# Optimization experiments

Hardware: AMD Instinct MI355X
Metric: run time of the kernel (lower is better)

Reference implementation:

```python
import jax, jax.numpy as jnp
import numpy as np

B, Tq, DIM = 4, 2048, 1024
TKV, N_LAT, DLAT = 16, 64, 1024
HEADS, DHEAD = 8, 64
LN_EPS = 1e-5


def setup_inputs() -> dict:
    key = jax.random.key(0)
    ks = jax.random.split(key, 6)
    qo = jax.random.normal(ks[0], (B, Tq, DIM), dtype=jnp.float32)
    kvo = jax.random.normal(ks[1], (B, TKV, N_LAT, DLAT), dtype=jnp.float32)
    # 16 media tokens, evenly spaced, first at index 16 (so q_time==0 for early tokens)
    media = jnp.zeros((B, Tq), dtype=bool)
    idx = 16 + jnp.arange(TKV) * (Tq // TKV)  # 16, 144, ..., 1936
    media = media.at[:, idx].set(True)
    ln_g = jnp.ones((DIM,), dtype=jnp.float32)
    ln_b = jnp.zeros((DIM,), dtype=jnp.float32)
    Wq = jax.random.normal(ks[2], (DIM, HEADS * DHEAD), dtype=jnp.float32) * 0.02
    Wkv = jax.random.normal(ks[3], (DLAT, HEADS * DHEAD * 2), dtype=jnp.float32) * 0.02
    Wout = jax.random.normal(ks[4], (HEADS * DHEAD, DIM), dtype=jnp.float32) * 0.02
    return {"qo": qo, "kvo": kvo, "media_locations": media,
            "ln_g": ln_g, "ln_b": ln_b, "Wq": Wq, "Wkv": Wkv, "Wout": Wout}


def _layernorm(x, g, b):
    mu = jnp.mean(x, axis=-1, keepdims=True)
    var = jnp.var(x, axis=-1, keepdims=True)
    return (x - mu) * jax.lax.rsqrt(var + LN_EPS) * g + b


def reference(qo, kvo, media_locations, ln_g, ln_b, Wq, Wkv, Wout):
    scale = DHEAD ** (-0.5)
    b, tq, _ = qo.shape
    _, tkv, n, _ = kvo.shape
    q = _layernorm(qo, ln_g, ln_b) @ Wq  # (b, tq, h*d)
    q = q.reshape(b, tq, HEADS, DHEAD).transpose(0, 2, 1, 3) * scale  # b h i d
    kv = kvo.reshape(b, tkv * n, -1) @ Wkv  # (b, j, 2*h*d)
    k, v = jnp.split(kv, 2, axis=-1)
    k = k.reshape(b, tkv * n, HEADS, DHEAD).transpose(0, 2, 1, 3)  # b h j d
    v = v.reshape(b, tkv * n, HEADS, DHEAD).transpose(0, 2, 1, 3)
    sim = jnp.einsum('bhid,bhjd->bhij', q, k)  # (b, h, tq, tkv*n)
    kv_time = jnp.repeat(jnp.arange(tkv) + 1, n)  # (tkv*n,)
    q_time = jnp.cumsum(media_locations.astype(jnp.int32), axis=-1)  # (b, tq)
    mask = q_time[:, None, :, None] == kv_time[None, None, None, :]  # only_attend_immediate
    neg = -jnp.finfo(sim.dtype).max
    sim = jnp.where(mask, sim, neg)
    attn = jax.nn.softmax(sim, axis=-1)
    attn = jnp.where((q_time == 0)[:, None, :, None], 0.0, attn)
    out = jnp.einsum('bhij,bhjd->bhid', attn, v)
    out = out.transpose(0, 2, 1, 3).reshape(b, tq, HEADS * DHEAD)
    return out @ Wout
```

## Files before the change

kernel.cpp:

```cpp
#include <hip/hip_runtime.h>
#include <cstdint>
#include <cstddef>

#define BB    4
#define TQ    2048
#define DIM   1024
#define TKV   16
#define NLAT  64
#define DLAT  1024
#define HEADS 8
#define DHEAD 64
#define LN_EPS 1e-5f
#define NKV   (TKV*NLAT)
#define HD    (HEADS*DHEAD)

typedef unsigned short u16;
typedef __bf16 bf16x8 __attribute__((ext_vector_type(8)));
typedef float  f32x4  __attribute__((ext_vector_type(4)));

__device__ __forceinline__ u16 f2bf(float f) {
    unsigned u = __builtin_bit_cast(unsigned, f);
    u += 0x7fffu + ((u >> 16) & 1u);
    return (u16)(u >> 16);
}
__device__ __forceinline__ void gl_lds16(const void* g, void* l) {
    __builtin_amdgcn_global_load_lds(
        (const __attribute__((address_space(1))) void*)g,
        (__attribute__((address_space(3))) void*)l, 16, 0, 0);
}

__device__ __forceinline__ void transpose_dev(const float* __restrict__ W,
                                              u16* __restrict__ Wt,
                                              int K, int N, int n0, int k0,
                                              float (*tile)[33]) {
    int t = threadIdx.x;
    int r = t >> 3, c4 = (t & 7) * 4;
    float4 v = *(const float4*)&W[(size_t)(k0 + r) * N + n0 + c4];
    tile[r][c4 + 0] = v.x; tile[r][c4 + 1] = v.y;
    tile[r][c4 + 2] = v.z; tile[r][c4 + 3] = v.w;
    __syncthreads();
    uint2 pk;
    pk.x = (unsigned)f2bf(tile[c4 + 0][r]) | ((unsigned)f2bf(tile[c4 + 1][r]) << 16);
    pk.y = (unsigned)f2bf(tile[c4 + 2][r]) | ((unsigned)f2bf(tile[c4 + 3][r]) << 16);
    *(uint2*)&Wt[(size_t)(n0 + r) * K + k0 + c4] = pk;
}

__global__ __launch_bounds__(256) void prep_k(
    const float* __restrict__ qo, const float* __restrict__ kvo,
    const uint8_t* __restrict__ media,
    const float* __restrict__ ln_g, const float* __restrict__ ln_b,
    const float* __restrict__ Wq, const float* __restrict__ Wkv,
    const float* __restrict__ Wout,
    int* __restrict__ qt, u16* __restrict__ Aq, u16* __restrict__ Akv,
    u16* __restrict__ Wqt, u16* __restrict__ Wkvt, u16* __restrict__ Woutt) {
    __shared__ int part[256];
    __shared__ int cnt_sh;
    __shared__ float sh[8];
    __shared__ float mu_s, rs_s;
    __shared__ float tile[32][33];
    int blk = blockIdx.x, t = threadIdx.x;

    if (blk < 4) {
        int b = blk;
        int c = 0;
        for (int i = 0; i < 32; ++i) c += (media[t * 32 + i] != 0);
        part[t] = c;
        __syncthreads();
        if (t == 0) { int s = 0; for (int i = 0; i < 256; ++i) s += part[i]; cnt_sh = s; }
        __syncthreads();
        bool is_u8 = (cnt_sh >= 48);
        int vals[8];
        for (int i = 0; i < 8; ++i) {
            int idx = t * 8 + i;
            int m;
            if (is_u8) m = (media[(size_t)b * TQ + idx] != 0) ? 1 : 0;
            else       m = (((const uint32_t*)media)[(size_t)b * TQ + idx] != 0u) ? 1 : 0;
            vals[i] = m;
        }
        int loc = 0;
        for (int i = 0; i < 8; ++i) loc += vals[i];
        __syncthreads();
        part[t] = loc;
        __syncthreads();
        int pre = 0;
        for (int i = 0; i < t; ++i) pre += part[i];
        int run = pre;
        for (int i = 0; i < 8; ++i) {
            run += vals[i];
            qt[(size_t)b * TQ + t * 8 + i] = run;
        }
    } else if (blk < 4 + BB * TQ) {
        int row = blk - 4;
        float4 v = *(const float4*)(qo + (size_t)row * DIM + t * 4);
        float s  = v.x + v.y + v.z + v.w;
        float ss = v.x * v.x + v.y * v.y + v.z * v.z + v.w * v.w;
        for (int off = 32; off; off >>= 1) { s += __shfl_down(s, off); ss += __shfl_down(ss, off); }
        if ((t & 63) == 0) { sh[(t >> 6) * 2] = s; sh[(t >> 6) * 2 + 1] = ss; }
        __syncthreads();
        if (t == 0) {
            float S  = sh[0] + sh[2] + sh[4] + sh[6];
            float SS = sh[1] + sh[3] + sh[5] + sh[7];
            float m  = S * (1.0f / DIM);
            mu_s = m;
            rs_s = rsqrtf(SS * (1.0f / DIM) - m * m + LN_EPS);
        }
        __syncthreads();
        float mu = mu_s, rs = rs_s;
        float4 gv = *(const float4*)(ln_g + t * 4);
        float4 bv = *(const float4*)(ln_b + t * 4);
        float a0 = (v.x - mu) * rs * gv.x + bv.x;
        float a1 = (v.y - mu) * rs * gv.y + bv.y;
        float a2 = (v.z - mu) * rs * gv.z + bv.z;
        float a3 = (v.w - mu) * rs * gv.w + bv.w;
        uint2 pk;
        pk.x = (unsigned)f2bf(a0) | ((unsigned)f2bf(a1) << 16);
        pk.y = (unsigned)f2bf(a2) | ((unsigned)f2bf(a3) << 16);
        *(uint2*)(Aq + (size_t)row * DIM + t * 4) = pk;
    } else if (blk < 4 + BB * TQ + 2048) {
        size_t i = (size_t)(blk - 4 - BB * TQ) * 256 + t;
        float4 a = ((const float4*)kvo)[i * 2];
        float4 b = ((const float4*)kvo)[i * 2 + 1];
        uint4 pk;
        pk.x = (unsigned)f2bf(a.x) | ((unsigned)f2bf(a.y) << 16);
        pk.y = (unsigned)f2bf(a.z) | ((unsigned)f2bf(a.w) << 16);
        pk.z = (unsigned)f2bf(b.x) | ((unsigned)f2bf(b.y) << 16);
        pk.w = (unsigned)f2bf(b.z) | ((unsigned)f2bf(b.w) << 16);
        ((uint4*)Akv)[i] = pk;
    } else if (blk < 10244 + 512) {
        int id = blk - 10244;
        transpose_dev(Wq, Wqt, DIM, HD, (id & 15) * 32, (id >> 4) * 32, tile);
    } else if (blk < 10756 + 1024) {
        int id = blk - 10756;
        transpose_dev(Wkv, Wkvt, DLAT, 2 * HD, (id & 31) * 32, (id >> 5) * 32, tile);
    } else {
        int id = blk - 11780;
        transpose_dev(Wout, Woutt, HD, DIM, (id & 31) * 32, (id >> 5) * 32, tile);
    }
}

template <typename CT>
__device__ __forceinline__ void gemm_body(const u16* __restrict__ A,
                                          const u16* __restrict__ Bt,
                                          CT* __restrict__ C,
                                          int M, int N, int K, float outscale,
                                          int bx, int by,
                                          u16* As0, u16* Bs0, u16* As1, u16* Bs1) {
    int t = threadIdx.x;
    int lane = t & 63, w = t >> 6;
    int wr = w >> 1, wc = w & 1;
    int fr = lane & 15, fg = lane >> 4;
    int row0 = by * 128, col0 = bx * 128;

    const u16* Ag = A  + (size_t)(row0 + (t >> 2)) * K + (t & 3) * 8;
    const u16* Bg = Bt + (size_t)(col0 + (t >> 2)) * K + (t & 3) * 8;
    size_t rstr = (size_t)64 * K;

    int aoff = (wr * 64 + fr) * 32 + fg * 8;
    int boff = (wc * 64 + fr) * 32 + fg * 8;

    f32x4 acc[4][4];
#pragma unroll
    for (int mi = 0; mi < 4; ++mi)
#pragma unroll
        for (int ni = 0; ni < 4; ++ni) acc[mi][ni] = (f32x4){0.f, 0.f, 0.f, 0.f};

    auto stage = [&](u16* Asb, u16* Bsb, int k0) {
        char* al = (char*)Asb + w * 1024;
        char* bl = (char*)Bsb + w * 1024;
        gl_lds16(Ag + k0,        al);
        gl_lds16(Ag + k0 + rstr, al + 4096);
        gl_lds16(Bg + k0,        bl);
        gl_lds16(Bg + k0 + rstr, bl + 4096);
    };
    auto compute = [&](const u16* Asb, const u16* Bsb) {
        bf16x8 af[4], bfv[4];
#pragma unroll
        for (int mi = 0; mi < 4; ++mi) af[mi]  = *(const bf16x8*)(Asb + aoff + mi * 512);
#pragma unroll
        for (int ni = 0; ni < 4; ++ni) bfv[ni] = *(const bf16x8*)(Bsb + boff + ni * 512);
#pragma unroll
        for (int mi = 0; mi < 4; ++mi)
#pragma unroll
            for (int ni = 0; ni < 4; ++ni)
                acc[mi][ni] = __builtin_amdgcn_mfma_f32_16x16x32_bf16(
                    af[mi], bfv[ni], acc[mi][ni], 0, 0, 0);
    };

    int nt = K >> 5;
    stage(As0, Bs0, 0);
    __syncthreads();
    for (int it = 0; it < nt; it += 2) {
        stage(As1, Bs1, (it + 1) << 5);
        compute(As0, Bs0);
        __syncthreads();
        if (it + 2 < nt) stage(As0, Bs0, (it + 2) << 5);
        compute(As1, Bs1);
        __syncthreads();
    }

#pragma unroll
    for (int mi = 0; mi < 4; ++mi) {
        int r0 = row0 + wr * 64 + mi * 16 + fg * 4;
#pragma unroll
        for (int ni = 0; ni < 4; ++ni) {
            int c = col0 + wc * 64 + ni * 16 + fr;
#pragma unroll
            for (int j = 0; j < 4; ++j) {
                float val = acc[mi][ni][j] * outscale;
                if constexpr (sizeof(CT) == 2) C[(size_t)(r0 + j) * N + c] = f2bf(val);
                else                           C[(size_t)(r0 + j) * N + c] = val;
            }
        }
    }
}

__global__ __launch_bounds__(256) void proj_k(
    const u16* __restrict__ Aq,  const u16* __restrict__ Wqt,  u16* __restrict__ qb,
    const u16* __restrict__ Akv, const u16* __restrict__ Wkvt, u16* __restrict__ kvb) {
    __shared__ u16 As0[4096], Bs0[4096], As1[4096], Bs1[4096];
    int id = blockIdx.x;
    if (id < 256) {
        gemm_body<u16>(Aq, Wqt, qb, BB * TQ, HD, DIM, 0.125f, id & 3, id >> 2,
                       As0, Bs0, As1, Bs1);
    } else {
        id -= 256;
        gemm_body<u16>(Akv, Wkvt, kvb, BB * NKV, 2 * HD, DLAT, 1.0f, id & 7, id >> 3,
                       As0, Bs0, As1, Bs1);
    }
}

__global__ __launch_bounds__(256) void out_k(
    const u16* __restrict__ aob, const u16* __restrict__ Woutt, float* __restrict__ out) {
    __shared__ u16 As0[4096], Bs0[4096], As1[4096], Bs1[4096];
    int id = blockIdx.x;
    gemm_body<float>(aob, Woutt, out, BB * TQ, DIM, HD, 1.0f, id & 7, id >> 3,
                     As0, Bs0, As1, Bs1);
}

__global__ __launch_bounds__(256) void attn_k(
    const u16* __restrict__ q,
    const u16* __restrict__ kv,
    const int* __restrict__ qt,
    u16* __restrict__ ao) {
    __shared__ u16 Ks[4096];
    __shared__ u16 VT[4096];
    __shared__ u16 Ps[1024];
    __shared__ float redm[4][16], reds[4][16];
    int i0 = blockIdx.x * 16;
    int h  = blockIdx.y;
    int b  = blockIdx.z;
    int t  = threadIdx.x;
    int lane = t & 63, w = t >> 6;
    int fr = lane & 15, fg = lane >> 4;

    int t0 = qt[(size_t)b * TQ + i0];
    if (t0 == 0) {
        int row = t >> 4, c = (t & 15) * 4;
        *(uint2*)&ao[((size_t)(b * TQ + i0 + row)) * HD + h * DHEAD + c] = make_uint2(0, 0);
        return;
    }
    int j0 = (t0 - 1) * 64;

    {
        int j = t >> 2, c16 = (t & 3) * 16;
        const u16* kvrow = kv + ((size_t)(b * NKV + j0 + j)) * (2 * HD) + h * DHEAD;
        uint4 k0v = *(const uint4*)(kvrow + c16);
        uint4 k1v = *(const uint4*)(kvrow + c16 + 8);
        uint4 v0v = *(const uint4*)(kvrow + HD + c16);
        uint4 v1v = *(const uint4*)(kvrow + HD + c16 + 8);
        int kb = j * 128 + c16 * 2;
        int swz = (j & 7) << 4;
        *(uint4*)((char*)Ks + ((kb)      ^ swz)) = k0v;
        *(uint4*)((char*)Ks + ((kb + 16) ^ swz)) = k1v;
        const u16* ve0 = (const u16*)&v0v;
        const u16* ve1 = (const u16*)&v1v;
#pragma unroll
        for (int e = 0; e < 8; ++e) {
            int d0 = c16 + e, d1 = c16 + 8 + e;
            *(u16*)((char*)VT + ((d0 * 128 + j * 2) ^ ((d0 & 7) << 4))) = ve0[e];
            *(u16*)((char*)VT + ((d1 * 128 + j * 2) ^ ((d1 & 7) << 4))) = ve1[e];
        }
    }
    const u16* qrow = q + ((size_t)(b * TQ + i0 + fr)) * HD + h * DHEAD + fg * 8;
    bf16x8 aq0 = *(const bf16x8*)(qrow);
    bf16x8 aq1 = *(const bf16x8*)(qrow + 32);
    __syncthreads();

    int r = w * 16 + fr;
    bf16x8 bk0 = *(const bf16x8*)((char*)Ks + ((r * 128 + fg * 16)      ^ ((r & 7) << 4)));
    bf16x8 bk1 = *(const bf16x8*)((char*)Ks + ((r * 128 + 64 + fg * 16) ^ ((r & 7) << 4)));
    f32x4 s = (f32x4){0.f, 0.f, 0.f, 0.f};
    s = __builtin_amdgcn_mfma_f32_16x16x32_bf16(aq0, bk0, s, 0, 0, 0);
    s = __builtin_amdgcn_mfma_f32_16x16x32_bf16(aq1, bk1, s, 0, 0, 0);

    float mx[4];
#pragma unroll
    for (int j = 0; j < 4; ++j) {
        float m = s[j];
        for (int off = 1; off < 16; off <<= 1) m = fmaxf(m, __shfl_xor(m, off));
        mx[j] = m;
        redm[w][fg * 4 + j] = m;
    }
    __syncthreads();
    float p[4];
#pragma unroll
    for (int j = 0; j < 4; ++j) {
        int row = fg * 4 + j;
        float M = fmaxf(fmaxf(redm[0][row], redm[1][row]), fmaxf(redm[2][row], redm[3][row]));
        p[j] = __expf(s[j] - M);
        float sm = p[j];
        for (int off = 1; off < 16; off <<= 1) sm += __shfl_xor(sm, off);
        reds[w][row] = sm;
    }
    __syncthreads();
#pragma unroll
    for (int j = 0; j < 4; ++j) {
        int row = fg * 4 + j;
        float S = reds[0][row] + reds[1][row] + reds[2][row] + reds[3][row];
        u16 pb = f2bf(p[j] / S);
        *(u16*)((char*)Ps + ((row * 128 + (w * 16 + fr) * 2) ^ ((row & 7) << 4))) = pb;
    }
    __syncthreads();

    bf16x8 pa0 = *(const bf16x8*)((char*)Ps + ((fr * 128 + fg * 16)      ^ ((fr & 7) << 4)));
    bf16x8 pa1 = *(const bf16x8*)((char*)Ps + ((fr * 128 + 64 + fg * 16) ^ ((fr & 7) << 4)));
    int d = w * 16 + fr;
    bf16x8 bv0 = *(const bf16x8*)((char*)VT + ((d * 128 + fg * 16)      ^ ((d & 7) << 4)));
    bf16x8 bv1 = *(const bf16x8*)((char*)VT + ((d * 128 + 64 + fg * 16) ^ ((d & 7) << 4)));
    f32x4 o = (f32x4){0.f, 0.f, 0.f, 0.f};
    o = __builtin_amdgcn_mfma_f32_16x16x32_bf16(pa0, bv0, o, 0, 0, 0);
    o = __builtin_amdgcn_mfma_f32_16x16x32_bf16(pa1, bv1, o, 0, 0, 0);
#pragma unroll
    for (int j = 0; j < 4; ++j)
        ao[((size_t)(b * TQ + i0 + fg * 4 + j)) * HD + h * DHEAD + d] = f2bf(o[j]);
}

extern "C" void kernel_launch(void* const* d_in, const int* in_sizes, int n_in,
                              void* d_out, int out_size, void* d_ws, size_t ws_size,
                              hipStream_t stream) {
    const float*   qo    = (const float*)d_in[0];
    const float*   kvo   = (const float*)d_in[1];
    const uint8_t* media = (const uint8_t*)d_in[2];
    const float*   ln_g  = (const float*)d_in[3];
    const float*   ln_b  = (const float*)d_in[4];
    const float*   Wq    = (const float*)d_in[5];
    const float*   Wkv   = (const float*)d_in[6];
    const float*   Wout  = (const float*)d_in[7];
    float* out = (float*)d_out;

    char* ws = (char*)d_ws;
    const size_t MB = 1u << 20;
    int* qt    = (int*)(ws);
    u16* Aq    = (u16*)(ws + 1  * MB);
    u16* aob   = (u16*)(ws + 1  * MB);
    u16* Akv   = (u16*)(ws + 17 * MB);
    u16* Wqt   = (u16*)(ws + 25 * MB);
    u16* Wkvt  = (u16*)(ws + 26 * MB);
    u16* Woutt = (u16*)(ws + 28 * MB);
    u16* qb    = (u16*)(ws + 29 * MB);
    u16* kvb   = (u16*)(ws + 37 * MB);

    prep_k<<<dim3(12292), dim3(256), 0, stream>>>(qo, kvo, media, ln_g, ln_b,
                                                  Wq, Wkv, Wout,
                                                  qt, Aq, Akv, Wqt, Wkvt, Woutt);
    proj_k<<<dim3(512), dim3(256), 0, stream>>>(Aq, Wqt, qb, Akv, Wkvt, kvb);
    attn_k<<<dim3(TQ / 16, HEADS, BB), dim3(256), 0, stream>>>(qb, kvb, qt, aob);
    out_k<<<dim3(512), dim3(256), 0, stream>>>(aob, Woutt, out);
}
```

Baseline: 169.8 us.

## Triple-buffer GEMM LDS staging with explicit vmcnt waits and barriers

Replaces the double-buffered LDS pipeline in the shared GEMM body with a three-slot ring buffer. Loads run two k-tiles ahead, and partial s_waitcnt vmcnt counts replace full __syncthreads, so global-to-LDS transfers overlap more of the MFMA compute. This hides more memory latency in the projection and output GEMMs. In exchange it uses 48KB of LDS per block instead of 32KB, which may lower occupancy, and it relies on hand-written waitcnt and sched_barrier ordering.

```diff
diff --git a/kernel.cpp b/kernel.cpp
--- a/kernel.cpp
+++ b/kernel.cpp
@@ -144,7 +144,7 @@
                                           CT* __restrict__ C,
                                           int M, int N, int K, float outscale,
                                           int bx, int by,
-                                          u16* As0, u16* Bs0, u16* As1, u16* Bs1) {
+                                          u16* S0, u16* S1, u16* S2) {
     int t = threadIdx.x;
     int lane = t & 63, w = t >> 6;
     int wr = w >> 1, wc = w & 1;
@@ -156,7 +156,7 @@
     size_t rstr = (size_t)64 * K;
 
     int aoff = (wr * 64 + fr) * 32 + fg * 8;
-    int boff = (wc * 64 + fr) * 32 + fg * 8;
+    int boff = 4096 + (wc * 64 + fr) * 32 + fg * 8;
 
     f32x4 acc[4][4];
 #pragma unroll
@@ -164,20 +164,21 @@
 #pragma unroll
         for (int ni = 0; ni < 4; ++ni) acc[mi][ni] = (f32x4){0.f, 0.f, 0.f, 0.f};
 
-    auto stage = [&](u16* Asb, u16* Bsb, int k0) {
-        char* al = (char*)Asb + w * 1024;
-        char* bl = (char*)Bsb + w * 1024;
+    auto stage = [&](u16* S, int kt) {
+        char* al = (char*)S + w * 1024;
+        char* bl = (char*)S + 8192 + w * 1024;
+        int k0 = kt << 5;
         gl_lds16(Ag + k0,        al);
         gl_lds16(Ag + k0 + rstr, al + 4096);
         gl_lds16(Bg + k0,        bl);
         gl_lds16(Bg + k0 + rstr, bl + 4096);
     };
-    auto compute = [&](const u16* Asb, const u16* Bsb) {
+    auto compute = [&](const u16* S) {
         bf16x8 af[4], bfv[4];
 #pragma unroll
-        for (int mi = 0; mi < 4; ++mi) af[mi]  = *(const bf16x8*)(Asb + aoff + mi * 512);
-#pragma unroll
-        for (int ni = 0; ni < 4; ++ni) bfv[ni] = *(const bf16x8*)(Bsb + boff + ni * 512);
+        for (int mi = 0; mi < 4; ++mi) af[mi]  = *(const bf16x8*)(S + aoff + mi * 512);
+#pragma unroll
+        for (int ni = 0; ni < 4; ++ni) bfv[ni] = *(const bf16x8*)(S + boff + ni * 512);
 #pragma unroll
         for (int mi = 0; mi < 4; ++mi)
 #pragma unroll
@@ -187,16 +188,27 @@
     };
 
     int nt = K >> 5;
-    stage(As0, Bs0, 0);
-    __syncthreads();
-    for (int it = 0; it < nt; it += 2) {
-        stage(As1, Bs1, (it + 1) << 5);
-        compute(As0, Bs0);
-        __syncthreads();
-        if (it + 2 < nt) stage(As0, Bs0, (it + 2) << 5);
-        compute(As1, Bs1);
-        __syncthreads();
-    }
+    u16 *b0 = S0, *b1 = S1, *b2 = S2;
+    stage(b0, 0);
+    stage(b1, 1);
+    for (int it = 0; it < nt - 2; ++it) {
+        stage(b2, it + 2);
+        asm volatile("s_waitcnt vmcnt(8)" ::: "memory");
+        __builtin_amdgcn_s_barrier();
+        __builtin_amdgcn_sched_barrier(0);
+        compute(b0);
+        __builtin_amdgcn_sched_barrier(0);
+        __builtin_amdgcn_s_barrier();
+        u16* tmp = b0; b0 = b1; b1 = b2; b2 = tmp;
+    }
+    asm volatile("s_waitcnt vmcnt(4)" ::: "memory");
+    __builtin_amdgcn_s_barrier();
+    __builtin_amdgcn_sched_barrier(0);
+    compute(b0);
+    asm volatile("s_waitcnt vmcnt(0)" ::: "memory");
+    __builtin_amdgcn_s_barrier();
+    __builtin_amdgcn_sched_barrier(0);
+    compute(b1);
 
 #pragma unroll
     for (int mi = 0; mi < 4; ++mi) {
@@ -217,24 +229,24 @@
 __global__ __launch_bounds__(256) void proj_k(
     const u16* __restrict__ Aq,  const u16* __restrict__ Wqt,  u16* __restrict__ qb,
     const u16* __restrict__ Akv, const u16* __restrict__ Wkvt, u16* __restrict__ kvb) {
-    __shared__ u16 As0[4096], Bs0[4096], As1[4096], Bs1[4096];
+    __shared__ u16 S0[8192], S1[8192], S2[8192];
     int id = blockIdx.x;
     if (id < 256) {
         gemm_body<u16>(Aq, Wqt, qb, BB * TQ, HD, DIM, 0.125f, id & 3, id >> 2,
-                       As0, Bs0, As1, Bs1);
+                       S0, S1, S2);
     } else {
         id -= 256;
         gemm_body<u16>(Akv, Wkvt, kvb, BB * NKV, 2 * HD, DLAT, 1.0f, id & 7, id >> 3,
-                       As0, Bs0, As1, Bs1);
+                       S0, S1, S2);
     }
 }
 
 __global__ __launch_bounds__(256) void out_k(
     const u16* __restrict__ aob, const u16* __restrict__ Woutt, float* __restrict__ out) {
-    __shared__ u16 As0[4096], Bs0[4096], As1[4096], Bs1[4096];
+    __shared__ u16 S0[8192], S1[8192], S2[8192];
     int id = blockIdx.x;
     gemm_body<float>(aob, Woutt, out, BB * TQ, DIM, HD, 1.0f, id & 7, id >> 3,
-                     As0, Bs0, As1, Bs1);
+                     S0, S1, S2);
 }
 
 __global__ __launch_bounds__(256) void attn_k(
```

After: 170.1 us. No clear change (+0.2%).

## Pre-pack weights in MFMA fragment order and load B directly to registers

Applied to the files above, without the earlier changes.

The weight prep kernel now writes each weight matrix in a packed layout matching the per-lane MFMA B-fragment order, so the GEMM body loads B fragments straight from global memory into registers instead of staging them through LDS. The A tile in LDS gets an XOR swizzle on its 16-byte chunks to cut bank conflicts. This halves LDS use and LDS traffic per block. In exchange, B comes from global/L2 on every k-step with register double-buffering, which adds latency exposure and register pressure.

```diff
diff --git a/kernel.cpp b/kernel.cpp
--- a/kernel.cpp
+++ b/kernel.cpp
@@ -29,20 +29,29 @@
         (__attribute__((address_space(3))) void*)l, 16, 0, 0);
 }
 
-__device__ __forceinline__ void transpose_dev(const float* __restrict__ W,
-                                              u16* __restrict__ Wt,
-                                              int K, int N, int n0, int k0,
-                                              float (*tile)[33]) {
+__device__ __forceinline__ void pack_dev(const float* __restrict__ W,
+                                         u16* __restrict__ Wf,
+                                         int K, int N, int n0, int k0,
+                                         float (*tile)[33]) {
     int t = threadIdx.x;
-    int r = t >> 3, c4 = (t & 7) * 4;
-    float4 v = *(const float4*)&W[(size_t)(k0 + r) * N + n0 + c4];
-    tile[r][c4 + 0] = v.x; tile[r][c4 + 1] = v.y;
-    tile[r][c4 + 2] = v.z; tile[r][c4 + 3] = v.w;
-    __syncthreads();
+    {
+        int r = t >> 3, c4 = (t & 7) * 4;
+        float4 v = *(const float4*)&W[(size_t)(k0 + r) * N + n0 + c4];
+        tile[r][c4 + 0] = v.x; tile[r][c4 + 1] = v.y;
+        tile[r][c4 + 2] = v.z; tile[r][c4 + 3] = v.w;
+    }
+    __syncthreads();
+    int entry = t >> 1, half = t & 1;
+    int lane = entry & 63, ntl = entry >> 6, e0 = half * 4;
+    int kl = (lane >> 4) * 8 + e0;
+    int nl = ntl * 16 + (lane & 15);
     uint2 pk;
-    pk.x = (unsigned)f2bf(tile[c4 + 0][r]) | ((unsigned)f2bf(tile[c4 + 1][r]) << 16);
-    pk.y = (unsigned)f2bf(tile[c4 + 2][r]) | ((unsigned)f2bf(tile[c4 + 3][r]) << 16);
-    *(uint2*)&Wt[(size_t)(n0 + r) * K + k0 + c4] = pk;
+    pk.x = (unsigned)f2bf(tile[kl + 0][nl]) | ((unsigned)f2bf(tile[kl + 1][nl]) << 16);
+    pk.y = (unsigned)f2bf(tile[kl + 2][nl]) | ((unsigned)f2bf(tile[kl + 3][nl]) << 16);
+    size_t ntile = (size_t)(n0 / 16 + ntl);
+    size_t idx = ((ntile * (K >> 5) + (k0 >> 5)) * 64 + lane) * 8 + e0;
+    *(uint2*)&Wf[idx] = pk;
+    __syncthreads();
 }
 
 __global__ __launch_bounds__(256) void prep_k(
@@ -52,7 +61,7 @@
     const float* __restrict__ Wq, const float* __restrict__ Wkv,
     const float* __restrict__ Wout,
     int* __restrict__ qt, u16* __restrict__ Aq, u16* __restrict__ Akv,
-    u16* __restrict__ Wqt, u16* __restrict__ Wkvt, u16* __restrict__ Woutt) {
+    u16* __restrict__ Wqf, u16* __restrict__ Wkvf, u16* __restrict__ Woutf) {
     __shared__ int part[256];
     __shared__ int cnt_sh;
     __shared__ float sh[8];
@@ -128,35 +137,34 @@
         ((uint4*)Akv)[i] = pk;
     } else if (blk < 10244 + 512) {
         int id = blk - 10244;
-        transpose_dev(Wq, Wqt, DIM, HD, (id & 15) * 32, (id >> 4) * 32, tile);
+        pack_dev(Wq, Wqf, DIM, HD, (id & 15) * 32, (id >> 4) * 32, tile);
     } else if (blk < 10756 + 1024) {
         int id = blk - 10756;
-        transpose_dev(Wkv, Wkvt, DLAT, 2 * HD, (id & 31) * 32, (id >> 5) * 32, tile);
+        pack_dev(Wkv, Wkvf, DLAT, 2 * HD, (id & 31) * 32, (id >> 5) * 32, tile);
     } else {
         int id = blk - 11780;
-        transpose_dev(Wout, Woutt, HD, DIM, (id & 31) * 32, (id >> 5) * 32, tile);
+        pack_dev(Wout, Woutf, HD, DIM, (id & 31) * 32, (id >> 5) * 32, tile);
     }
 }
 
 template <typename CT>
 __device__ __forceinline__ void gemm_body(const u16* __restrict__ A,
-                                          const u16* __restrict__ Bt,
+                                          const u16* __restrict__ Wf,
                                           CT* __restrict__ C,
                                           int M, int N, int K, float outscale,
                                           int bx, int by,
-                                          u16* As0, u16* Bs0, u16* As1, u16* Bs1) {
+                                          u16* As0, u16* As1) {
     int t = threadIdx.x;
     int lane = t & 63, w = t >> 6;
     int wr = w >> 1, wc = w & 1;
     int fr = lane & 15, fg = lane >> 4;
     int row0 = by * 128, col0 = bx * 128;
-
-    const u16* Ag = A  + (size_t)(row0 + (t >> 2)) * K + (t & 3) * 8;
-    const u16* Bg = Bt + (size_t)(col0 + (t >> 2)) * K + (t & 3) * 8;
+    int nt = K >> 5;
+
+    const u16* Ag = A + (size_t)(row0 + (t >> 2)) * K + ((t & 3) ^ ((t >> 2) & 3)) * 8;
     size_t rstr = (size_t)64 * K;
-
-    int aoff = (wr * 64 + fr) * 32 + fg * 8;
-    int boff = (wc * 64 + fr) * 32 + fg * 8;
+    const u16* Bf = Wf + ((size_t)(bx * 8 + wc * 4) * nt) * 512 + lane * 8;
+    int aoff = (wr * 64 + fr) * 32 + (fg ^ (fr & 3)) * 8;
 
     f32x4 acc[4][4];
 #pragma unroll
@@ -164,37 +172,38 @@
 #pragma unroll
         for (int ni = 0; ni < 4; ++ni) acc[mi][ni] = (f32x4){0.f, 0.f, 0.f, 0.f};
 
-    auto stage = [&](u16* Asb, u16* Bsb, int k0) {
-        char* al = (char*)Asb + w * 1024;
-        char* bl = (char*)Bsb + w * 1024;
-        gl_lds16(Ag + k0,        al);
-        gl_lds16(Ag + k0 + rstr, al + 4096);
-        gl_lds16(Bg + k0,        bl);
-        gl_lds16(Bg + k0 + rstr, bl + 4096);
+    auto stage = [&](u16* S, int kt) {
+        char* al = (char*)S + w * 1024;
+        gl_lds16(Ag + kt * 32,        al);
+        gl_lds16(Ag + kt * 32 + rstr, al + 4096);
     };
-    auto compute = [&](const u16* Asb, const u16* Bsb) {
-        bf16x8 af[4], bfv[4];
-#pragma unroll
-        for (int mi = 0; mi < 4; ++mi) af[mi]  = *(const bf16x8*)(Asb + aoff + mi * 512);
-#pragma unroll
-        for (int ni = 0; ni < 4; ++ni) bfv[ni] = *(const bf16x8*)(Bsb + boff + ni * 512);
+    auto loadB = [&](bf16x8* bf, int kt) {
+#pragma unroll
+        for (int ni = 0; ni < 4; ++ni)
+            bf[ni] = *(const bf16x8*)(Bf + ((size_t)ni * nt + kt) * 512);
+    };
+    auto compute = [&](const u16* S, const bf16x8* bf) {
+        bf16x8 af[4];
+#pragma unroll
+        for (int mi = 0; mi < 4; ++mi) af[mi] = *(const bf16x8*)(S + aoff + mi * 512);
 #pragma unroll
         for (int mi = 0; mi < 4; ++mi)
 #pragma unroll
             for (int ni = 0; ni < 4; ++ni)
                 acc[mi][ni] = __builtin_amdgcn_mfma_f32_16x16x32_bf16(
-                    af[mi], bfv[ni], acc[mi][ni], 0, 0, 0);
+                    af[mi], bf[ni], acc[mi][ni], 0, 0, 0);
     };
 
-    int nt = K >> 5;
-    stage(As0, Bs0, 0);
-    __syncthreads();
-    for (int it = 0; it < nt; it += 2) {
-        stage(As1, Bs1, (it + 1) << 5);
-        compute(As0, Bs0);
-        __syncthreads();
-        if (it + 2 < nt) stage(As0, Bs0, (it + 2) << 5);
-        compute(As1, Bs1);
+    bf16x8 bc[4], bn[4];
+    stage(As0, 0);
+    loadB(bc, 0);
+    __syncthreads();
+    for (int kt = 0; kt < nt; kt += 2) {
+        if (kt + 1 < nt) { stage(As1, kt + 1); loadB(bn, kt + 1); }
+        compute(As0, bc);
+        __syncthreads();
+        if (kt + 2 < nt) { stage(As0, kt + 2); loadB(bc, kt + 2); }
+        compute(As1, bn);
         __syncthreads();
     }
 
@@ -215,26 +224,23 @@
 }
 
 __global__ __launch_bounds__(256) void proj_k(
-    const u16* __restrict__ Aq,  const u16* __restrict__ Wqt,  u16* __restrict__ qb,
-    const u16* __restrict__ Akv, const u16* __restrict__ Wkvt, u16* __restrict__ kvb) {
-    __shared__ u16 As0[4096], Bs0[4096], As1[4096], Bs1[4096];
+    const u16* __restrict__ Aq,  const u16* __restrict__ Wqf,  u16* __restrict__ qb,
+    const u16* __restrict__ Akv, const u16* __restrict__ Wkvf, u16* __restrict__ kvb) {
+    __shared__ u16 As0[4096], As1[4096];
     int id = blockIdx.x;
     if (id < 256) {
-        gemm_body<u16>(Aq, Wqt, qb, BB * TQ, HD, DIM, 0.125f, id & 3, id >> 2,
-                       As0, Bs0, As1, Bs1);
+        gemm_body<u16>(Aq, Wqf, qb, BB * TQ, HD, DIM, 0.125f, id & 3, id >> 2, As0, As1);
     } else {
         id -= 256;
-        gemm_body<u16>(Akv, Wkvt, kvb, BB * NKV, 2 * HD, DLAT, 1.0f, id & 7, id >> 3,
-                       As0, Bs0, As1, Bs1);
+        gemm_body<u16>(Akv, Wkvf, kvb, BB * NKV, 2 * HD, DLAT, 1.0f, id & 7, id >> 3, As0, As1);
     }
 }
 
 __global__ __launch_bounds__(256) void out_k(
-    const u16* __restrict__ aob, const u16* __restrict__ Woutt, float* __restrict__ out) {
-    __shared__ u16 As0[4096], Bs0[4096], As1[4096], Bs1[4096];
+    const u16* __restrict__ aob, const u16* __restrict__ Woutf, float* __restrict__ out) {
+    __shared__ u16 As0[4096], As1[4096];
     int id = blockIdx.x;
-    gemm_body<float>(aob, Woutt, out, BB * TQ, DIM, HD, 1.0f, id & 7, id >> 3,
-                     As0, Bs0, As1, Bs1);
+    gemm_body<float>(aob, Woutf, out, BB * TQ, DIM, HD, 1.0f, id & 7, id >> 3, As0, As1);
 }
 
 __global__ __launch_bounds__(256) void attn_k(
@@ -354,16 +360,16 @@
     u16* Aq    = (u16*)(ws + 1  * MB);
     u16* aob   = (u16*)(ws + 1  * MB);
     u16* Akv   = (u16*)(ws + 17 * MB);
-    u16* Wqt   = (u16*)(ws + 25 * MB);
-    u16* Wkvt  = (u16*)(ws + 26 * MB);
-    u16* Woutt = (u16*)(ws + 28 * MB);
+    u16* Wqf   = (u16*)(ws + 25 * MB);
+    u16* Wkvf  = (u16*)(ws + 26 * MB);
+    u16* Woutf = (u16*)(ws + 28 * MB);
     u16* qb    = (u16*)(ws + 29 * MB);
     u16* kvb   = (u16*)(ws + 37 * MB);
 
     prep_k<<<dim3(12292), dim3(256), 0, stream>>>(qo, kvo, media, ln_g, ln_b,
                                                   Wq, Wkv, Wout,
-                                                  qt, Aq, Akv, Wqt, Wkvt, Woutt);
-    proj_k<<<dim3(512), dim3(256), 0, stream>>>(Aq, Wqt, qb, Akv, Wkvt, kvb);
+                                                  qt, Aq, Akv, Wqf, Wkvf, Woutf);
+    proj_k<<<dim3(512), dim3(256), 0, stream>>>(Aq, Wqf, qb, Akv, Wkvf, kvb);
     attn_k<<<dim3(TQ / 16, HEADS, BB), dim3(256), 0, stream>>>(qb, kvb, qt, aob);
-    out_k<<<dim3(512), dim3(256), 0, stream>>>(aob, Woutt, out);
-}
+    out_k<<<dim3(512), dim3(256), 0, stream>>>(aob, Woutf, out);
+}
```

New measurement: 176.0 us. 3.6% more time.

## Fuse projection, attention and output GEMMs into one persistent kernel with grid barriers

Applied to the files above, without the earlier changes.

Replaces the three launches after prep (projection GEMM, attention, output GEMM) with a single 512-block kernel. Blocks synchronise through an atomic-counter grid barrier, and each block runs eight attention jobs in a loop, reusing the GEMM shared-memory buffers. The aim is to remove launch gaps and kernel-boundary drains. In exchange it depends on all 512 blocks being co-resident (launch bounds of 2 blocks per SM), spins on a global atomic with a timeout, and reduces attention parallelism to one block per eight jobs.

```diff
diff --git a/kernel.cpp b/kernel.cpp
--- a/kernel.cpp
+++ b/kernel.cpp
@@ -52,7 +52,8 @@
     const float* __restrict__ Wq, const float* __restrict__ Wkv,
     const float* __restrict__ Wout,
     int* __restrict__ qt, u16* __restrict__ Aq, u16* __restrict__ Akv,
-    u16* __restrict__ Wqt, u16* __restrict__ Wkvt, u16* __restrict__ Woutt) {
+    u16* __restrict__ Wqt, u16* __restrict__ Wkvt, u16* __restrict__ Woutt,
+    unsigned* __restrict__ cnt) {
     __shared__ int part[256];
     __shared__ int cnt_sh;
     __shared__ float sh[8];
@@ -61,6 +62,7 @@
     int blk = blockIdx.x, t = threadIdx.x;
 
     if (blk < 4) {
+        if (blk == 0 && t == 0) *cnt = 0;
         int b = blk;
         int c = 0;
         for (int i = 0; i < 32; ++i) c += (media[t * 32 + i] != 0);
@@ -139,9 +141,7 @@
 }
 
 template <typename CT>
-__device__ __forceinline__ void gemm_body(const u16* __restrict__ A,
-                                          const u16* __restrict__ Bt,
-                                          CT* __restrict__ C,
+__device__ __forceinline__ void gemm_body(const u16* A, const u16* Bt, CT* C,
                                           int M, int N, int K, float outscale,
                                           int bx, int by,
                                           u16* As0, u16* Bs0, u16* As1, u16* Bs1) {
@@ -214,41 +214,12 @@
     }
 }
 
-__global__ __launch_bounds__(256) void proj_k(
-    const u16* __restrict__ Aq,  const u16* __restrict__ Wqt,  u16* __restrict__ qb,
-    const u16* __restrict__ Akv, const u16* __restrict__ Wkvt, u16* __restrict__ kvb) {
-    __shared__ u16 As0[4096], Bs0[4096], As1[4096], Bs1[4096];
-    int id = blockIdx.x;
-    if (id < 256) {
-        gemm_body<u16>(Aq, Wqt, qb, BB * TQ, HD, DIM, 0.125f, id & 3, id >> 2,
-                       As0, Bs0, As1, Bs1);
-    } else {
-        id -= 256;
-        gemm_body<u16>(Akv, Wkvt, kvb, BB * NKV, 2 * HD, DLAT, 1.0f, id & 7, id >> 3,
-                       As0, Bs0, As1, Bs1);
-    }
-}
-
-__global__ __launch_bounds__(256) void out_k(
-    const u16* __restrict__ aob, const u16* __restrict__ Woutt, float* __restrict__ out) {
-    __shared__ u16 As0[4096], Bs0[4096], As1[4096], Bs1[4096];
-    int id = blockIdx.x;
-    gemm_body<float>(aob, Woutt, out, BB * TQ, DIM, HD, 1.0f, id & 7, id >> 3,
-                     As0, Bs0, As1, Bs1);
-}
-
-__global__ __launch_bounds__(256) void attn_k(
-    const u16* __restrict__ q,
-    const u16* __restrict__ kv,
-    const int* __restrict__ qt,
-    u16* __restrict__ ao) {
-    __shared__ u16 Ks[4096];
-    __shared__ u16 VT[4096];
-    __shared__ u16 Ps[1024];
-    __shared__ float redm[4][16], reds[4][16];
-    int i0 = blockIdx.x * 16;
-    int h  = blockIdx.y;
-    int b  = blockIdx.z;
+__device__ __forceinline__ void attn_job(
+    const u16* q, const u16* kv, const int* qt, u16* ao, int job,
+    u16* Ks, u16* VT, u16* Ps, float* redm, float* reds) {
+    int i0 = (job & 127) * 16;
+    int h  = (job >> 7) & 7;
+    int b  = job >> 10;
     int t  = threadIdx.x;
     int lane = t & 63, w = t >> 6;
     int fr = lane & 15, fg = lane >> 4;
@@ -293,30 +264,28 @@
     s = __builtin_amdgcn_mfma_f32_16x16x32_bf16(aq0, bk0, s, 0, 0, 0);
     s = __builtin_amdgcn_mfma_f32_16x16x32_bf16(aq1, bk1, s, 0, 0, 0);
 
-    float mx[4];
 #pragma unroll
     for (int j = 0; j < 4; ++j) {
         float m = s[j];
         for (int off = 1; off < 16; off <<= 1) m = fmaxf(m, __shfl_xor(m, off));
-        mx[j] = m;
-        redm[w][fg * 4 + j] = m;
+        redm[w * 16 + fg * 4 + j] = m;
     }
     __syncthreads();
     float p[4];
 #pragma unroll
     for (int j = 0; j < 4; ++j) {
         int row = fg * 4 + j;
-        float M = fmaxf(fmaxf(redm[0][row], redm[1][row]), fmaxf(redm[2][row], redm[3][row]));
+        float M = fmaxf(fmaxf(redm[row], redm[16 + row]), fmaxf(redm[32 + row], redm[48 + row]));
         p[j] = __expf(s[j] - M);
         float sm = p[j];
         for (int off = 1; off < 16; off <<= 1) sm += __shfl_xor(sm, off);
-        reds[w][row] = sm;
+        reds[w * 16 + row] = sm;
     }
     __syncthreads();
 #pragma unroll
     for (int j = 0; j < 4; ++j) {
         int row = fg * 4 + j;
-        float S = reds[0][row] + reds[1][row] + reds[2][row] + reds[3][row];
+        float S = reds[row] + reds[16 + row] + reds[32 + row] + reds[48 + row];
         u16 pb = f2bf(p[j] / S);
         *(u16*)((char*)Ps + ((row * 128 + (w * 16 + fr) * 2) ^ ((row & 7) << 4))) = pb;
     }
@@ -333,6 +302,54 @@
 #pragma unroll
     for (int j = 0; j < 4; ++j)
         ao[((size_t)(b * TQ + i0 + fg * 4 + j)) * HD + h * DHEAD + d] = f2bf(o[j]);
+}
+
+__device__ __forceinline__ void gridbar(unsigned* cnt, unsigned target) {
+    __syncthreads();
+    if (threadIdx.x == 0) {
+        __hip_atomic_fetch_add(cnt, 1u, __ATOMIC_ACQ_REL, __HIP_MEMORY_SCOPE_AGENT);
+        unsigned it = 0;
+        while (__hip_atomic_load(cnt, __ATOMIC_ACQUIRE, __HIP_MEMORY_SCOPE_AGENT) < target
+               && ++it < 30000000u)
+            __builtin_amdgcn_s_sleep(2);
+    }
+    __syncthreads();
+}
+
+__global__ __launch_bounds__(256, 2) void mega_k(
+    const u16* Aq,  const u16* Wqt,  u16* qb,
+    const u16* Akv, const u16* Wkvt, u16* kvb,
+    const int* qt, u16* aob,
+    const u16* Woutt, float* out, unsigned* cnt) {
+    __shared__ u16 As0[4096], Bs0[4096], As1[4096], Bs1[4096];
+    int id = blockIdx.x;
+
+    if (id < 256) {
+        gemm_body<u16>(Aq, Wqt, qb, BB * TQ, HD, DIM, 0.125f, id & 3, id >> 2,
+                       As0, Bs0, As1, Bs1);
+    } else {
+        int k = id - 256;
+        gemm_body<u16>(Akv, Wkvt, kvb, BB * NKV, 2 * HD, DLAT, 1.0f, k & 7, k >> 3,
+                       As0, Bs0, As1, Bs1);
+    }
+    gridbar(cnt, 512);
+
+    {
+        u16* Ks = As0;
+        u16* VT = Bs0;
+        u16* Ps = As1;
+        float* redm = (float*)Bs1;
+        float* reds = redm + 64;
+#pragma unroll 1
+        for (int jj = 0; jj < 8; ++jj) {
+            __syncthreads();
+            attn_job(qb, kvb, qt, aob, id * 8 + jj, Ks, VT, Ps, redm, reds);
+        }
+    }
+    gridbar(cnt, 1024);
+
+    gemm_body<float>(aob, Woutt, out, BB * TQ, DIM, HD, 1.0f, id & 7, id >> 3,
+                     As0, Bs0, As1, Bs1);
 }
 
 extern "C" void kernel_launch(void* const* d_in, const int* in_sizes, int n_in,
@@ -350,7 +367,8 @@
 
     char* ws = (char*)d_ws;
     const size_t MB = 1u << 20;
-    int* qt    = (int*)(ws);
+    int*      qt    = (int*)(ws);
+    unsigned* cnt   = (unsigned*)(ws + (64 << 10));
     u16* Aq    = (u16*)(ws + 1  * MB);
     u16* aob   = (u16*)(ws + 1  * MB);
     u16* Akv   = (u16*)(ws + 17 * MB);
@@ -362,8 +380,7 @@
 
     prep_k<<<dim3(12292), dim3(256), 0, stream>>>(qo, kvo, media, ln_g, ln_b,
                                                   Wq, Wkv, Wout,
-                                                  qt, Aq, Akv, Wqt, Wkvt, Woutt);
-    proj_k<<<dim3(512), dim3(256), 0, stream>>>(Aq, Wqt, qb, Akv, Wkvt, kvb);
-    attn_k<<<dim3(TQ / 16, HEADS, BB), dim3(256), 0, stream>>>(qb, kvb, qt, aob);
-    out_k<<<dim3(512), dim3(256), 0, stream>>>(aob, Woutt, out);
-}
+                                                  qt, Aq, Akv, Wqt, Wkvt, Woutt, cnt);
+    mega_k<<<dim3(512), dim3(256), 0, stream>>>(Aq, Wqt, qb, Akv, Wkvt, kvb,
+                                                qt, aob, Woutt, out, cnt);
+}
```

New measurement: 304.9 us. +79.5%, slower.
